# Optimization experiments

Measured on AMD Instinct MI355X. Metric: run time of the kernel, lower is better.

Reference implementation:

```python
import jax, jax.numpy as jnp
import numpy as np

N_NODES = 102600
T = 64             # timesteps looped over by the LSTMCell
F_IN = 5           # LSTMCell input size
H = 64             # hidden / GAT channel dim
N_EDGES = 16 * N_NODES


def setup_inputs() -> dict:
    key = jax.random.key(0)
    ks = jax.random.split(key, 12)
    s = 0.1
    return {
        "x": jax.random.normal(ks[0], (N_NODES, T, F_IN), jnp.float32),
        "W_ih": jax.random.normal(ks[1], (4 * H, F_IN), jnp.float32) * s,
        "W_hh": jax.random.normal(ks[2], (4 * H, H), jnp.float32) * s,
        "b_ih": jax.random.normal(ks[3], (4 * H,), jnp.float32) * s,
        "b_hh": jax.random.normal(ks[4], (4 * H,), jnp.float32) * s,
        "gat_w": jax.random.normal(ks[5], (H, H), jnp.float32) * s,
        "att_src": jax.random.normal(ks[6], (H,), jnp.float32) * s,
        "att_dst": jax.random.normal(ks[7], (H,), jnp.float32) * s,
        "gat_bias": jax.random.normal(ks[8], (H,), jnp.float32) * s,
        "fc_w": jax.random.normal(ks[9], (1, H), jnp.float32) * s,
        "fc_b": jax.random.normal(ks[10], (1,), jnp.float32) * s,
        "edge_index": jax.random.randint(ks[11], (2, N_EDGES), 0, N_NODES, dtype=jnp.int64),
    }


def reference(x, W_ih, W_hh, b_ih, b_hh, gat_w, att_src, att_dst, gat_bias, fc_w, fc_b, edge_index):
    N = x.shape[0]
    h0 = jnp.zeros((N, H), x.dtype)
    c0 = jnp.zeros((N, H), x.dtype)

    # --- per-timestep LSTMCell recurrence (torch gate order: i, f, g, o) ---
    def step(carry, xt):
        h, c = carry
        gates = xt @ W_ih.T + b_ih + h @ W_hh.T + b_hh  # [N, 4H]
        i, f, g, o = jnp.split(gates, 4, axis=-1)
        c = jax.nn.sigmoid(f) * c + jax.nn.sigmoid(i) * jnp.tanh(g)
        h = jax.nn.sigmoid(o) * jnp.tanh(c)
        return (h, c), None

    (h, _), _ = jax.lax.scan(step, (h0, c0), jnp.swapaxes(x, 0, 1))  # scan over T

    # --- GATConv(64, 64), heads=1, add_self_loops=True, negative_slope=0.2 ---
    xp = h @ gat_w.T                                   # [N, H] transformed features
    loops = jnp.arange(N, dtype=edge_index.dtype)
    src = jnp.concatenate([edge_index[0], loops])      # message source j
    dst = jnp.concatenate([edge_index[1], loops])      # message target i
    a_src = xp @ att_src                               # [N]
    a_dst = xp @ att_dst                               # [N]
    alpha = jax.nn.leaky_relu(a_src[src] + a_dst[dst], 0.2)  # [E+N]
    # segment softmax over incoming edges per dst node
    amax = jax.ops.segment_max(alpha, dst, num_segments=N)
    ae = jnp.exp(alpha - amax[dst])
    denom = jax.ops.segment_sum(ae, dst, num_segments=N)
    ae = ae / denom[dst]
    out = jax.ops.segment_sum(ae[:, None] * xp[src], dst, num_segments=N) + gat_bias

    # --- fc: Linear(64, 1) + LeakyReLU (default slope 0.01) ---
    return jax.nn.leaky_relu(out @ fc_w.T + fc_b, 0.01)
```

## Files before the change

### kernel.cpp

```cpp
#include <hip/hip_runtime.h>
#include <cstdint>
#include <cstddef>

#define T_STEPS 64
#define F_INP 5
#define LOG2E 1.44269504088896340736f

typedef _Float16 f16x8 __attribute__((ext_vector_type(8)));
typedef float f32x4 __attribute__((ext_vector_type(4)));

__device__ __forceinline__ float leaky(float x, float s){ return x>0.f? x : s*x; }
__device__ __forceinline__ float rcpf(float x){ return __builtin_amdgcn_rcpf(x); }
__device__ __forceinline__ float exp2fast(float x){ return __builtin_amdgcn_exp2f(x); }

__global__ __launch_bounds__(256, 4) void lstm_mfma(
    const float* __restrict__ x, const float* __restrict__ W_ih,
    const float* __restrict__ W_hh, const float* __restrict__ b_ih,
    const float* __restrict__ b_hh, const float* __restrict__ vcomb,
    float2* __restrict__ asx, float* __restrict__ a_dst,
    float* __restrict__ denom, float* __restrict__ oacc, int N)
{
  __shared__ __align__(16) _Float16 Hs0[32][64];
  __shared__ __align__(16) _Float16 Hs1[32][64];
  __shared__ __align__(16) _Float16 Xs0[32][8];
  __shared__ __align__(16) _Float16 Xs1[32][8];
  __shared__ __align__(16) _Float16 Zero8[8];
  __shared__ __align__(16) float    Hf[32][65];

  const int tid   = threadIdx.x;
  const int lane  = tid & 63;
  const int wq    = tid >> 6;
  const int col16 = lane & 15;
  const int grp   = lane >> 4;
  const int base  = blockIdx.x * 32;

  f16x8 Bh[4][2], Bx[4];
  #pragma unroll
  for (int n=0;n<4;n++){
    const float sc = (n==2) ? 2.f*LOG2E : LOG2E;
    const int gate = n*64 + wq*16 + col16;
    #pragma unroll
    for (int kk=0;kk<2;kk++){
      const float* p = W_hh + gate*64 + kk*32 + grp*8;
      #pragma unroll
      for (int e=0;e<8;e++) Bh[n][kk][e] = (_Float16)(p[e]*sc);
    }
    f16x8 bx = {0,0,0,0,0,0,0,0};
    if (grp==0){
      #pragma unroll
      for (int e=0;e<5;e++) bx[e] = (_Float16)(W_ih[gate*5+e]*sc);
      bx[5] = (_Float16)((b_ih[gate]+b_hh[gate])*sc);
    }
    Bx[n] = bx;
  }

  ((float4*)&Hs0[0][0])[tid] = float4{0.f,0.f,0.f,0.f};
  if (tid==0) ((float4*)Zero8)[0] = float4{0.f,0.f,0.f,0.f};

  const int  xn5  = tid/5, xe5 = tid - xn5*5;
  const bool xact = (tid < 160);
  const int  gxnode = base + xn5;
  const bool xlive  = xact && (gxnode < N);
  const float* xptr = x + (size_t)(xlive ? gxnode : 0)*(T_STEPS*F_INP) + xe5 + F_INP;
  if (xact){
    float v0 = xlive ? x[(size_t)gxnode*(T_STEPS*F_INP) + xe5] : 0.f;
    Xs0[xn5][xe5] = (_Float16)v0;
  }
  if (tid < 32){
    Xs0[tid][5]=(_Float16)1.f; Xs0[tid][6]=(_Float16)0.f; Xs0[tid][7]=(_Float16)0.f;
    Xs1[tid][5]=(_Float16)1.f; Xs1[tid][6]=(_Float16)0.f; Xs1[tid][7]=(_Float16)0.f;
  }

  const int sw = (col16&7)<<3;
  int roff0[2], roff1[2], xoffm[2], soff[2][4];
  const int j = wq*16 + col16;
  #pragma unroll
  for (int m=0;m<2;m++){
    const int nodeA = 16*m + col16;
    roff0[m] = nodeA*64 + ((grp*8) ^ sw);
    roff1[m] = nodeA*64 + ((32 + grp*8) ^ sw);
    xoffm[m] = nodeA*8;
    #pragma unroll
    for (int r=0;r<4;r++){
      const int node = 16*m + 4*grp + r;
      soff[m][r] = node*64 + (j ^ ((4*(grp&1)+r)<<3));
    }
  }

  float creg[2][4];
  #pragma unroll
  for (int m=0;m<2;m++)
    #pragma unroll
    for (int r=0;r<4;r++) creg[m][r]=0.f;

  __syncthreads();

#define LSTM_STEP(HC, HN, XC, XN, XOFF, LAST) {                                \
    float xval = 0.f;                                                          \
    if (!(LAST) && xlive) xval = xptr[XOFF];                                   \
    f32x4 AC0[2], AC1[2], AC2[2], AC3[2];                                      \
    _Pragma("unroll")                                                          \
    for (int m=0;m<2;m++){                                                     \
      f16x8 a0 = *(const f16x8*)(&HC[0][0] + roff0[m]);                        \
      f16x8 a1 = *(const f16x8*)(&HC[0][0] + roff1[m]);                        \
      const _Float16* px = (grp==0) ? (&XC[0][0] + xoffm[m]) : Zero8;          \
      f16x8 ax = *(const f16x8*)px;                                            \
      f32x4 z4 = f32x4{0.f,0.f,0.f,0.f};                                       \
      f32x4 c0=z4, c1=z4, c2=z4, c3=z4;                                        \
      c0 = __builtin_amdgcn_mfma_f32_16x16x32_f16(a0, Bh[0][0], c0, 0,0,0);    \
      c1 = __builtin_amdgcn_mfma_f32_16x16x32_f16(a0, Bh[1][0], c1, 0,0,0);    \
      c2 = __builtin_amdgcn_mfma_f32_16x16x32_f16(a0, Bh[2][0], c2, 0,0,0);    \
      c3 = __builtin_amdgcn_mfma_f32_16x16x32_f16(a0, Bh[3][0], c3, 0,0,0);    \
      c0 = __builtin_amdgcn_mfma_f32_16x16x32_f16(a1, Bh[0][1], c0, 0,0,0);    \
      c1 = __builtin_amdgcn_mfma_f32_16x16x32_f16(a1, Bh[1][1], c1, 0,0,0);    \
      c2 = __builtin_amdgcn_mfma_f32_16x16x32_f16(a1, Bh[2][1], c2, 0,0,0);    \
      c3 = __builtin_amdgcn_mfma_f32_16x16x32_f16(a1, Bh[3][1], c3, 0,0,0);    \
      c0 = __builtin_amdgcn_mfma_f32_16x16x32_f16(ax, Bx[0],    c0, 0,0,0);    \
      c1 = __builtin_amdgcn_mfma_f32_16x16x32_f16(ax, Bx[1],    c1, 0,0,0);    \
      c2 = __builtin_amdgcn_mfma_f32_16x16x32_f16(ax, Bx[2],    c2, 0,0,0);    \
      c3 = __builtin_amdgcn_mfma_f32_16x16x32_f16(ax, Bx[3],    c3, 0,0,0);    \
      AC0[m]=c0; AC1[m]=c1; AC2[m]=c2; AC3[m]=c3;                              \
    }                                                                          \
    _Pragma("unroll")                                                          \
    for (int m=0;m<2;m++){                                                     \
      _Pragma("unroll")                                                        \
      for (int r=0;r<4;r++){                                                   \
        float e_i = exp2fast(-AC0[m][r]);                                      \
        float e_f = exp2fast(-AC1[m][r]);                                      \
        float zg2 = fminf(AC2[m][r], 60.f);                                    \
        float e_g = exp2fast(zg2);                                             \
        float e_o = exp2fast(-AC3[m][r]);                                      \
        float Ag = (1.f+e_i)*(1.f+e_g);                                        \
        float Bf = 1.f+e_f;                                                    \
        float rD = rcpf(Ag*Bf);                                                \
        float cn = (creg[m][r]*Ag + (e_g-1.f)*Bf)*rD;                          \
        creg[m][r] = cn;                                                       \
        float c2v = fminf(cn*(2.f*LOG2E), 120.f);                              \
        float e_c = exp2fast(c2v);                                             \
        float hv = (e_c-1.f)*rcpf((1.f+e_o)*(1.f+e_c));                        \
        if (LAST){                                                             \
          Hf[16*m+4*grp+r][j] = hv;                                            \
        } else {                                                               \
          (&HN[0][0])[soff[m][r]] = (_Float16)hv;                              \
        }                                                                      \
      }                                                                        \
    }                                                                          \
    if (!(LAST) && xact) XN[xn5][xe5] = (_Float16)xval;                        \
  }

  for (int tt=0; tt<T_STEPS/2; ++tt){
    LSTM_STEP(Hs0, Hs1, Xs0, Xs1, 0, false);
    __syncthreads();
    LSTM_STEP(Hs1, Hs0, Xs1, Xs0, F_INP, (tt==T_STEPS/2-1));
    __syncthreads();
    xptr += 2*F_INP;
  }
#undef LSTM_STEP

  const int en = tid >> 3, es = tid & 7;
  const int gn2 = base + en;
  float as=0.f, ad=0.f, xf=0.f;
  #pragma unroll
  for (int q=0;q<8;q++){
    float hv = Hf[en][es*8+q];
    as = fmaf(hv, vcomb[es*8+q],     as);
    ad = fmaf(hv, vcomb[64+es*8+q],  ad);
    xf = fmaf(hv, vcomb[128+es*8+q], xf);
  }
  #pragma unroll
  for (int off=1; off<8; off<<=1){
    as += __shfl_xor(as, off);
    ad += __shfl_xor(ad, off);
    xf += __shfl_xor(xf, off);
  }
  if (es==0 && gn2 < N){
    asx[gn2]   = float2{as, xf};
    a_dst[gn2] = ad;
    denom[gn2] = 0.f;
    oacc[gn2]  = 0.f;
  }
}

__global__ void gat_setup(const int* __restrict__ ei,
                          const float* __restrict__ gat_w,
                          const float* __restrict__ att_src,
                          const float* __restrict__ att_dst,
                          const float* __restrict__ fc_w,
                          const float* __restrict__ gat_bias,
                          const float* __restrict__ fc_b,
                          float* __restrict__ vcomb,
                          unsigned* __restrict__ mode)
{
  int j = threadIdx.x;
  unsigned long long nz = __ballot(ei[2*j+1] != 0);
  float bdp = gat_bias[j]*fc_w[j];
  #pragma unroll
  for (int off=32; off; off>>=1) bdp += __shfl_down(bdp, off);
  if (j==0){
    *mode = (nz==0ULL) ? 1u : 0u;
    vcomb[192] = bdp + fc_b[0];
  }
  float va=0.f, vd=0.f, vf=0.f;
  #pragma unroll 8
  for (int k=0;k<64;k++){
    float g = gat_w[k*64+j];
    va += att_src[k]*g;
    vd += att_dst[k]*g;
    vf += fc_w[k]*g;
  }
  vcomb[j]=va; vcomb[64+j]=vd; vcomb[128+j]=vf;
}

__device__ __forceinline__ void load_edge(const int* ei, unsigned mode,
                                          long long e, long long E,
                                          int& s, int& d)
{
  if (e>=E){ s=d=(int)(e-E); }
  else if (mode){
    const long long* e64 = (const long long*)ei;
    s=(int)e64[e]; d=(int)e64[E+e];
  } else {
    s=ei[e]; d=ei[E+e];
  }
}

__global__ __launch_bounds__(256) void edge_pass(
    const int* __restrict__ ei, const unsigned* __restrict__ mode_p,
    const float2* __restrict__ asx, const float* __restrict__ a_dst,
    float* __restrict__ denom, float* __restrict__ oacc,
    long long E, long long total)
{
  long long e = (long long)blockIdx.x*256 + threadIdx.x;
  if (e>=total) return;
  int s,d;
  load_edge(ei, *mode_p, e, E, s, d);
  float2 sv = asx[s];
  float al = leaky(sv.x + a_dst[d], 0.2f);
  float ew = __expf(al);
  atomicAdd(&denom[d], ew);
  atomicAdd(&oacc[d], ew * sv.y);
}

__global__ __launch_bounds__(256) void finalize(
    const float* __restrict__ oacc, const float* __restrict__ denom,
    const float* __restrict__ vcomb, float* __restrict__ out, int N)
{
  int n = blockIdx.x*256+threadIdx.x;
  if (n>=N) return;
  float v = oacc[n] * rcpf(denom[n]) + vcomb[192];
  out[n] = leaky(v, 0.01f);
}

extern "C" void kernel_launch(void* const* d_in, const int* in_sizes, int n_in,
                              void* d_out, int out_size, void* d_ws, size_t ws_size,
                              hipStream_t stream)
{
  const float* x      = (const float*)d_in[0];
  const float* W_ih   = (const float*)d_in[1];
  const float* W_hh   = (const float*)d_in[2];
  const float* b_ih   = (const float*)d_in[3];
  const float* b_hh   = (const float*)d_in[4];
  const float* gat_w  = (const float*)d_in[5];
  const float* att_s  = (const float*)d_in[6];
  const float* att_d  = (const float*)d_in[7];
  const float* gat_b  = (const float*)d_in[8];
  const float* fc_w   = (const float*)d_in[9];
  const float* fc_b   = (const float*)d_in[10];
  const int*   ei     = (const int*)d_in[11];

  const int N = in_sizes[0]/(T_STEPS*F_INP);
  const long long E = in_sizes[11]/2;
  const long long total = E + N;

  float* ws = (float*)d_ws;
  size_t off = 0;
  float2* asx    = (float2*)(ws + off); off += (size_t)2*N;
  float* a_dst   = ws + off; off += (size_t)N;
  float* denom   = ws + off; off += (size_t)N;
  float* oacc    = ws + off; off += (size_t)N;
  float* vcomb   = ws + off; off += 256;
  unsigned* mode = (unsigned*)(ws + off); off += 1;

  gat_setup<<<1,64,0,stream>>>(ei, gat_w, att_s, att_d, fc_w, gat_b, fc_b, vcomb, mode);

  lstm_mfma<<<dim3((N+31)/32), dim3(256), 0, stream>>>(
      x, W_ih, W_hh, b_ih, b_hh, vcomb, asx, a_dst, denom, oacc, N);

  int eb = (int)((total+255)/256);
  edge_pass<<<dim3(eb), dim3(256), 0, stream>>>(ei, mode, asx, a_dst, denom, oacc, E, total);

  finalize<<<dim3((N+255)/256), dim3(256), 0, stream>>>(oacc, denom, vcomb, (float*)d_out, N);
}
```

Measured before the change: 650.6 us.

## Move half of LSTM weight fragments to LDS to raise occupancy

Keeps only the first K-half of the W_hh MFMA B-fragments in registers. The second half and the input/bias fragments are staged once into shared memory and reloaded every timestep. The launch bound rises from 4 to 5 waves per SIMD, and gate math is interleaved per m-tile so fewer accumulators stay live. The final hidden state goes through registers and is overlaid on the weight LDS buffer after an extra barrier. The aim is more resident blocks to hide the latency of the serial recurrence, at the cost of extra LDS reads per step and higher LDS use per block.

Result: slower. 722.9 us (+11.1%).

```diff
diff --git a/kernel.cpp b/kernel.cpp
--- a/kernel.cpp
+++ b/kernel.cpp
@@ -13,7 +13,9 @@
 __device__ __forceinline__ float rcpf(float x){ return __builtin_amdgcn_rcpf(x); }
 __device__ __forceinline__ float exp2fast(float x){ return __builtin_amdgcn_exp2f(x); }
 
-__global__ __launch_bounds__(256, 4) void lstm_mfma(
+#define MF(a,b,c) __builtin_amdgcn_mfma_f32_16x16x32_f16((a),(b),(c),0,0,0)
+
+__global__ __launch_bounds__(256, 5) void lstm_mfma(
     const float* __restrict__ x, const float* __restrict__ W_ih,
     const float* __restrict__ W_hh, const float* __restrict__ b_ih,
     const float* __restrict__ b_hh, const float* __restrict__ vcomb,
@@ -25,7 +27,8 @@
   __shared__ __align__(16) _Float16 Xs0[32][8];
   __shared__ __align__(16) _Float16 Xs1[32][8];
   __shared__ __align__(16) _Float16 Zero8[8];
-  __shared__ __align__(16) float    Hf[32][65];
+  __shared__ __align__(16) _Float16 BH1[8192];
+  __shared__ __align__(16) _Float16 BXI[2048];
 
   const int tid   = threadIdx.x;
   const int lane  = tid & 63;
@@ -34,24 +37,41 @@
   const int grp   = lane >> 4;
   const int base  = blockIdx.x * 32;
 
-  f16x8 Bh[4][2], Bx[4];
+  f16x8 Bh0[4];
   #pragma unroll
   for (int n=0;n<4;n++){
     const float sc = (n==2) ? 2.f*LOG2E : LOG2E;
     const int gate = n*64 + wq*16 + col16;
-    #pragma unroll
-    for (int kk=0;kk<2;kk++){
-      const float* p = W_hh + gate*64 + kk*32 + grp*8;
-      #pragma unroll
-      for (int e=0;e<8;e++) Bh[n][kk][e] = (_Float16)(p[e]*sc);
-    }
-    f16x8 bx = {0,0,0,0,0,0,0,0};
-    if (grp==0){
-      #pragma unroll
-      for (int e=0;e<5;e++) bx[e] = (_Float16)(W_ih[gate*5+e]*sc);
-      bx[5] = (_Float16)((b_ih[gate]+b_hh[gate])*sc);
-    }
-    Bx[n] = bx;
+    const float* p = W_hh + gate*64 + grp*8;
+    #pragma unroll
+    for (int e=0;e<8;e++) Bh0[n][e] = (_Float16)(p[e]*sc);
+  }
+
+  #pragma unroll
+  for (int it=0; it<4; ++it){
+    const int idx = it*256 + tid;
+    const int n   = idx >> 8;
+    const int wqi = (idx >> 6) & 3;
+    const int l   = idx & 63;
+    const float sc = (n==2) ? 2.f*LOG2E : LOG2E;
+    const int gate = n*64 + wqi*16 + (l & 15);
+    const float* p = W_hh + gate*64 + 32 + (l>>4)*8;
+    f16x8 v;
+    #pragma unroll
+    for (int e=0;e<8;e++) v[e] = (_Float16)(p[e]*sc);
+    *(f16x8*)&BH1[idx*8] = v;
+  }
+  {
+    const int n   = tid >> 6;
+    const int wqi = (tid >> 4) & 3;
+    const int l   = tid & 15;
+    const float sc = (n==2) ? 2.f*LOG2E : LOG2E;
+    const int gate = n*64 + wqi*16 + l;
+    f16x8 v = {0,0,0,0,0,0,0,0};
+    #pragma unroll
+    for (int e=0;e<5;e++) v[e] = (_Float16)(W_ih[gate*5+e]*sc);
+    v[5] = (_Float16)((b_ih[gate]+b_hh[gate])*sc);
+    *(f16x8*)&BXI[tid*8] = v;
   }
 
   ((float4*)&Hs0[0][0])[tid] = float4{0.f,0.f,0.f,0.f};
@@ -71,23 +91,19 @@
     Xs1[tid][5]=(_Float16)1.f; Xs1[tid][6]=(_Float16)0.f; Xs1[tid][7]=(_Float16)0.f;
   }
 
-  const int sw = (col16&7)<<3;
-  int roff0[2], roff1[2], xoffm[2], soff[2][4];
-  const int j = wq*16 + col16;
-  #pragma unroll
-  for (int m=0;m<2;m++){
-    const int nodeA = 16*m + col16;
-    roff0[m] = nodeA*64 + ((grp*8) ^ sw);
-    roff1[m] = nodeA*64 + ((32 + grp*8) ^ sw);
-    xoffm[m] = nodeA*8;
-    #pragma unroll
-    for (int r=0;r<4;r++){
-      const int node = 16*m + 4*grp + r;
-      soff[m][r] = node*64 + (j ^ ((4*(grp&1)+r)<<3));
-    }
-  }
+  const int sw    = (col16&7)<<3;
+  const int roff0 = col16*64 + ((grp*8) ^ sw);
+  const int roff1 = roff0 ^ 32;
+  const int xoff0 = col16*8;
+  const int j     = wq*16 + col16;
+  const int jg    = j ^ ((grp&1)<<5);
+  const int sb    = 4*grp*64;
+  const _Float16* bh1p = BH1 + (wq*64 + lane)*8;
+  const _Float16* bxip = (lane<16) ? (BXI + (wq*16 + lane)*8) : Zero8;
+  const int bxstep = (lane<16) ? 512 : 0;
 
   float creg[2][4];
+  float hreg[2][4];
   #pragma unroll
   for (int m=0;m<2;m++)
     #pragma unroll
@@ -98,38 +114,35 @@
 #define LSTM_STEP(HC, HN, XC, XN, XOFF, LAST) {                                \
     float xval = 0.f;                                                          \
     if (!(LAST) && xlive) xval = xptr[XOFF];                                   \
-    f32x4 AC0[2], AC1[2], AC2[2], AC3[2];                                      \
+    f16x8 s10 = *(const f16x8*)(bh1p);                                         \
+    f16x8 s11 = *(const f16x8*)(bh1p + 2048);                                  \
+    f16x8 s12 = *(const f16x8*)(bh1p + 4096);                                  \
+    f16x8 s13 = *(const f16x8*)(bh1p + 6144);                                  \
+    f16x8 sx0 = *(const f16x8*)(bxip);                                         \
+    f16x8 sx1 = *(const f16x8*)(bxip + bxstep);                                \
+    f16x8 sx2 = *(const f16x8*)(bxip + 2*bxstep);                              \
+    f16x8 sx3 = *(const f16x8*)(bxip + 2*bxstep + bxstep);                     \
     _Pragma("unroll")                                                          \
     for (int m=0;m<2;m++){                                                     \
-      f16x8 a0 = *(const f16x8*)(&HC[0][0] + roff0[m]);                        \
-      f16x8 a1 = *(const f16x8*)(&HC[0][0] + roff1[m]);                        \
-      const _Float16* px = (grp==0) ? (&XC[0][0] + xoffm[m]) : Zero8;          \
+      f16x8 a0 = *(const f16x8*)(&HC[0][0] + roff0 + m*1024);                  \
+      f16x8 a1 = *(const f16x8*)(&HC[0][0] + roff1 + m*1024);                  \
+      const _Float16* px = (grp==0) ? (&XC[0][0] + xoff0 + m*128) : Zero8;     \
       f16x8 ax = *(const f16x8*)px;                                            \
       f32x4 z4 = f32x4{0.f,0.f,0.f,0.f};                                       \
       f32x4 c0=z4, c1=z4, c2=z4, c3=z4;                                        \
-      c0 = __builtin_amdgcn_mfma_f32_16x16x32_f16(a0, Bh[0][0], c0, 0,0,0);    \
-      c1 = __builtin_amdgcn_mfma_f32_16x16x32_f16(a0, Bh[1][0], c1, 0,0,0);    \
-      c2 = __builtin_amdgcn_mfma_f32_16x16x32_f16(a0, Bh[2][0], c2, 0,0,0);    \
-      c3 = __builtin_amdgcn_mfma_f32_16x16x32_f16(a0, Bh[3][0], c3, 0,0,0);    \
-      c0 = __builtin_amdgcn_mfma_f32_16x16x32_f16(a1, Bh[0][1], c0, 0,0,0);    \
-      c1 = __builtin_amdgcn_mfma_f32_16x16x32_f16(a1, Bh[1][1], c1, 0,0,0);    \
-      c2 = __builtin_amdgcn_mfma_f32_16x16x32_f16(a1, Bh[2][1], c2, 0,0,0);    \
-      c3 = __builtin_amdgcn_mfma_f32_16x16x32_f16(a1, Bh[3][1], c3, 0,0,0);    \
-      c0 = __builtin_amdgcn_mfma_f32_16x16x32_f16(ax, Bx[0],    c0, 0,0,0);    \
-      c1 = __builtin_amdgcn_mfma_f32_16x16x32_f16(ax, Bx[1],    c1, 0,0,0);    \
-      c2 = __builtin_amdgcn_mfma_f32_16x16x32_f16(ax, Bx[2],    c2, 0,0,0);    \
-      c3 = __builtin_amdgcn_mfma_f32_16x16x32_f16(ax, Bx[3],    c3, 0,0,0);    \
-      AC0[m]=c0; AC1[m]=c1; AC2[m]=c2; AC3[m]=c3;                              \
-    }                                                                          \
-    _Pragma("unroll")                                                          \
-    for (int m=0;m<2;m++){                                                     \
+      c0 = MF(a0, Bh0[0], c0); c1 = MF(a0, Bh0[1], c1);                        \
+      c2 = MF(a0, Bh0[2], c2); c3 = MF(a0, Bh0[3], c3);                        \
+      c0 = MF(a1, s10, c0);    c1 = MF(a1, s11, c1);                           \
+      c2 = MF(a1, s12, c2);    c3 = MF(a1, s13, c3);                           \
+      c0 = MF(ax, sx0, c0);    c1 = MF(ax, sx1, c1);                           \
+      c2 = MF(ax, sx2, c2);    c3 = MF(ax, sx3, c3);                           \
       _Pragma("unroll")                                                        \
       for (int r=0;r<4;r++){                                                   \
-        float e_i = exp2fast(-AC0[m][r]);                                      \
-        float e_f = exp2fast(-AC1[m][r]);                                      \
-        float zg2 = fminf(AC2[m][r], 60.f);                                    \
+        float e_i = exp2fast(-c0[r]);                                          \
+        float e_f = exp2fast(-c1[r]);                                          \
+        float zg2 = fminf(c2[r], 60.f);                                        \
         float e_g = exp2fast(zg2);                                             \
-        float e_o = exp2fast(-AC3[m][r]);                                      \
+        float e_o = exp2fast(-c3[r]);                                          \
         float Ag = (1.f+e_i)*(1.f+e_g);                                        \
         float Bf = 1.f+e_f;                                                    \
         float rD = rcpf(Ag*Bf);                                                \
@@ -139,9 +152,9 @@
         float e_c = exp2fast(c2v);                                             \
         float hv = (e_c-1.f)*rcpf((1.f+e_o)*(1.f+e_c));                        \
         if (LAST){                                                             \
-          Hf[16*m+4*grp+r][j] = hv;                                            \
+          hreg[m][r] = hv;                                                     \
         } else {                                                               \
-          (&HN[0][0])[soff[m][r]] = (_Float16)hv;                              \
+          (&HN[0][0])[sb + m*1024 + r*64 + (jg ^ (r<<3))] = (_Float16)hv;      \
         }                                                                      \
       }                                                                        \
     }                                                                          \
@@ -157,12 +170,20 @@
   }
 #undef LSTM_STEP
 
+  float* HfOv = (float*)BH1;
+  #pragma unroll
+  for (int m=0;m<2;m++)
+    #pragma unroll
+    for (int r=0;r<4;r++)
+      HfOv[(16*m + 4*grp + r)*65 + j] = hreg[m][r];
+  __syncthreads();
+
   const int en = tid >> 3, es = tid & 7;
   const int gn2 = base + en;
   float as=0.f, ad=0.f, xf=0.f;
   #pragma unroll
   for (int q=0;q<8;q++){
-    float hv = Hf[en][es*8+q];
+    float hv = HfOv[en*65 + es*8 + q];
     as = fmaf(hv, vcomb[es*8+q],     as);
     ad = fmaf(hv, vcomb[64+es*8+q],  ad);
     xf = fmaf(hv, vcomb[128+es*8+q], xf);
```

## Interleave softmax accumulators and fuse per-row gate math into MFMA loop

Applied to the files above, without the earlier changes.

The separate denom and oacc arrays are merged into one interleaved float2 array. The two atomics per edge then hit the same cache line, and finalize does a single 8-byte load. The LSTM step also computes the gate nonlinearities right after each row-block's MFMAs instead of buffering all accumulators first. That lowers register pressure and may let the first block's transcendental math overlap the second block's MFMAs.

Measured after the change: 648.9 us. No clear change (-0.3%).

```diff
diff --git a/kernel.cpp b/kernel.cpp
--- a/kernel.cpp
+++ b/kernel.cpp
@@ -12,13 +12,15 @@
 __device__ __forceinline__ float leaky(float x, float s){ return x>0.f? x : s*x; }
 __device__ __forceinline__ float rcpf(float x){ return __builtin_amdgcn_rcpf(x); }
 __device__ __forceinline__ float exp2fast(float x){ return __builtin_amdgcn_exp2f(x); }
+
+#define MF(a,b,c) __builtin_amdgcn_mfma_f32_16x16x32_f16((a),(b),(c),0,0,0)
 
 __global__ __launch_bounds__(256, 4) void lstm_mfma(
     const float* __restrict__ x, const float* __restrict__ W_ih,
     const float* __restrict__ W_hh, const float* __restrict__ b_ih,
     const float* __restrict__ b_hh, const float* __restrict__ vcomb,
     float2* __restrict__ asx, float* __restrict__ a_dst,
-    float* __restrict__ denom, float* __restrict__ oacc, int N)
+    float2* __restrict__ da, int N)
 {
   __shared__ __align__(16) _Float16 Hs0[32][64];
   __shared__ __align__(16) _Float16 Hs1[32][64];
@@ -98,7 +100,6 @@
 #define LSTM_STEP(HC, HN, XC, XN, XOFF, LAST) {                                \
     float xval = 0.f;                                                          \
     if (!(LAST) && xlive) xval = xptr[XOFF];                                   \
-    f32x4 AC0[2], AC1[2], AC2[2], AC3[2];                                      \
     _Pragma("unroll")                                                          \
     for (int m=0;m<2;m++){                                                     \
       f16x8 a0 = *(const f16x8*)(&HC[0][0] + roff0[m]);                        \
@@ -107,29 +108,19 @@
       f16x8 ax = *(const f16x8*)px;                                            \
       f32x4 z4 = f32x4{0.f,0.f,0.f,0.f};                                       \
       f32x4 c0=z4, c1=z4, c2=z4, c3=z4;                                        \
-      c0 = __builtin_amdgcn_mfma_f32_16x16x32_f16(a0, Bh[0][0], c0, 0,0,0);    \
-      c1 = __builtin_amdgcn_mfma_f32_16x16x32_f16(a0, Bh[1][0], c1, 0,0,0);    \
-      c2 = __builtin_amdgcn_mfma_f32_16x16x32_f16(a0, Bh[2][0], c2, 0,0,0);    \
-      c3 = __builtin_amdgcn_mfma_f32_16x16x32_f16(a0, Bh[3][0], c3, 0,0,0);    \
-      c0 = __builtin_amdgcn_mfma_f32_16x16x32_f16(a1, Bh[0][1], c0, 0,0,0);    \
-      c1 = __builtin_amdgcn_mfma_f32_16x16x32_f16(a1, Bh[1][1], c1, 0,0,0);    \
-      c2 = __builtin_amdgcn_mfma_f32_16x16x32_f16(a1, Bh[2][1], c2, 0,0,0);    \
-      c3 = __builtin_amdgcn_mfma_f32_16x16x32_f16(a1, Bh[3][1], c3, 0,0,0);    \
-      c0 = __builtin_amdgcn_mfma_f32_16x16x32_f16(ax, Bx[0],    c0, 0,0,0);    \
-      c1 = __builtin_amdgcn_mfma_f32_16x16x32_f16(ax, Bx[1],    c1, 0,0,0);    \
-      c2 = __builtin_amdgcn_mfma_f32_16x16x32_f16(ax, Bx[2],    c2, 0,0,0);    \
-      c3 = __builtin_amdgcn_mfma_f32_16x16x32_f16(ax, Bx[3],    c3, 0,0,0);    \
-      AC0[m]=c0; AC1[m]=c1; AC2[m]=c2; AC3[m]=c3;                              \
-    }                                                                          \
-    _Pragma("unroll")                                                          \
-    for (int m=0;m<2;m++){                                                     \
+      c0 = MF(a0, Bh[0][0], c0); c1 = MF(a0, Bh[1][0], c1);                    \
+      c2 = MF(a0, Bh[2][0], c2); c3 = MF(a0, Bh[3][0], c3);                    \
+      c0 = MF(a1, Bh[0][1], c0); c1 = MF(a1, Bh[1][1], c1);                    \
+      c2 = MF(a1, Bh[2][1], c2); c3 = MF(a1, Bh[3][1], c3);                    \
+      c0 = MF(ax, Bx[0],    c0); c1 = MF(ax, Bx[1],    c1);                    \
+      c2 = MF(ax, Bx[2],    c2); c3 = MF(ax, Bx[3],    c3);                    \
       _Pragma("unroll")                                                        \
       for (int r=0;r<4;r++){                                                   \
-        float e_i = exp2fast(-AC0[m][r]);                                      \
-        float e_f = exp2fast(-AC1[m][r]);                                      \
-        float zg2 = fminf(AC2[m][r], 60.f);                                    \
+        float e_i = exp2fast(-c0[r]);                                          \
+        float e_f = exp2fast(-c1[r]);                                          \
+        float zg2 = fminf(c2[r], 60.f);                                        \
         float e_g = exp2fast(zg2);                                             \
-        float e_o = exp2fast(-AC3[m][r]);                                      \
+        float e_o = exp2fast(-c3[r]);                                          \
         float Ag = (1.f+e_i)*(1.f+e_g);                                        \
         float Bf = 1.f+e_f;                                                    \
         float rD = rcpf(Ag*Bf);                                                \
@@ -176,8 +167,7 @@
   if (es==0 && gn2 < N){
     asx[gn2]   = float2{as, xf};
     a_dst[gn2] = ad;
-    denom[gn2] = 0.f;
-    oacc[gn2]  = 0.f;
+    da[gn2]    = float2{0.f, 0.f};
   }
 }
 
@@ -227,7 +217,7 @@
 __global__ __launch_bounds__(256) void edge_pass(
     const int* __restrict__ ei, const unsigned* __restrict__ mode_p,
     const float2* __restrict__ asx, const float* __restrict__ a_dst,
-    float* __restrict__ denom, float* __restrict__ oacc,
+    float2* __restrict__ da,
     long long E, long long total)
 {
   long long e = (long long)blockIdx.x*256 + threadIdx.x;
@@ -237,18 +227,18 @@
   float2 sv = asx[s];
   float al = leaky(sv.x + a_dst[d], 0.2f);
   float ew = __expf(al);
-  atomicAdd(&denom[d], ew);
-  atomicAdd(&oacc[d], ew * sv.y);
+  atomicAdd(&da[d].x, ew);
+  atomicAdd(&da[d].y, ew * sv.y);
 }
 
 __global__ __launch_bounds__(256) void finalize(
-    const float* __restrict__ oacc, const float* __restrict__ denom,
-    const float* __restrict__ vcomb, float* __restrict__ out, int N)
+    const float2* __restrict__ da, const float* __restrict__ vcomb,
+    float* __restrict__ out, int N)
 {
   int n = blockIdx.x*256+threadIdx.x;
   if (n>=N) return;
-  float v = oacc[n] * rcpf(denom[n]) + vcomb[192];
-  out[n] = leaky(v, 0.01f);
+  float2 v = da[n];
+  out[n] = leaky(v.y * rcpf(v.x) + vcomb[192], 0.01f);
 }
 
 extern "C" void kernel_launch(void* const* d_in, const int* in_sizes, int n_in,
@@ -276,18 +266,17 @@
   size_t off = 0;
   float2* asx    = (float2*)(ws + off); off += (size_t)2*N;
   float* a_dst   = ws + off; off += (size_t)N;
-  float* denom   = ws + off; off += (size_t)N;
-  float* oacc    = ws + off; off += (size_t)N;
+  float2* da     = (float2*)(ws + off); off += (size_t)2*N;
   float* vcomb   = ws + off; off += 256;
   unsigned* mode = (unsigned*)(ws + off); off += 1;
 
   gat_setup<<<1,64,0,stream>>>(ei, gat_w, att_s, att_d, fc_w, gat_b, fc_b, vcomb, mode);
 
   lstm_mfma<<<dim3((N+31)/32), dim3(256), 0, stream>>>(
-      x, W_ih, W_hh, b_ih, b_hh, vcomb, asx, a_dst, denom, oacc, N);
+      x, W_ih, W_hh, b_ih, b_hh, vcomb, asx, a_dst, da, N);
 
   int eb = (int)((total+255)/256);
-  edge_pass<<<dim3(eb), dim3(256), 0, stream>>>(ei, mode, asx, a_dst, denom, oacc, E, total);
-
-  finalize<<<dim3((N+255)/256), dim3(256), 0, stream>>>(oacc, denom, vcomb, (float*)d_out, N);
-}
+  edge_pass<<<dim3(eb), dim3(256), 0, stream>>>(ei, mode, asx, a_dst, da, E, total);
+
+  finalize<<<dim3((N+255)/256), dim3(256), 0, stream>>>(da, vcomb, (float*)d_out, N);
+}
```
